# Kernel optimization log

Hardware: AMD Instinct MI355X
Metric: run time of the kernel (lower is better)

Reference implementation:

```python
import jax, jax.numpy as jnp
import numpy as np

D_K = 32  # hard-coded in original module


def setup_inputs() -> dict:
    key = jax.random.key(0)
    kq, kk, kv, km = jax.random.split(key, 4)
    B, H, S, D = 4, 12, 2048, D_K
    Q = jax.random.normal(kq, (B, H, S, D), dtype=jnp.float32)
    K = jax.random.normal(kk, (B, H, S, D), dtype=jnp.float32)
    V = jax.random.normal(kv, (B, H, S, D), dtype=jnp.float32)
    attn_mask = jax.random.bernoulli(km, 0.5, (B, H, S, S))
    return {"Q": Q, "K": K, "V": V, "attn_mask": attn_mask}


def tanh_max(a):
    # (exp(a) - exp(-a)) / sum_over_keys(exp(a) + exp(-a))
    ea = jnp.exp(a)
    ena = jnp.exp(-a)
    return (ea - ena) / (ea + ena).sum(axis=-1, keepdims=True)


def reference(Q, K, V, attn_mask):
    # scores: [B,H,S,S]
    scores = jnp.einsum("bhqd,bhkd->bhqk", Q, K) / np.sqrt(D_K).astype(np.float32)
    attn = tanh_max(scores)
    # NOTE: original calls attn.masked_fill(attn_mask, 0.0) WITHOUT assignment
    # (non-in-place), so the mask has no effect. Reproduced faithfully.
    context = jnp.einsum("bhqk,bhkd->bhqd", attn, V)
    return context
```

## Files before the change

### kernel.cpp

```cpp
#include <hip/hip_runtime.h>
#include <hip/hip_bf16.h>
#include <cstdint>
#include <cstddef>


#define SLEN 2048
#define DK   32
#define NBH  48
#define PROW 40

typedef __attribute__((ext_vector_type(8))) short bf16x8;
typedef __attribute__((ext_vector_type(4))) float f32x4;

__device__ __forceinline__ unsigned pk2(float a, float b) {
    __hip_bfloat162 h = __float22bfloat162_rn(make_float2(a, b));
    union { __hip_bfloat162 h2; unsigned u; } cv; cv.h2 = h; return cv.u;
}
__device__ __forceinline__ unsigned short f2b(float x) {
    __hip_bfloat16 h = __float2bfloat16(x);
    union { __hip_bfloat16 h; unsigned short u; } cv; cv.h = h; return cv.u;
}

__global__ __launch_bounds__(256)
void prep_vt(const float* __restrict__ V, unsigned short* __restrict__ VT) {
    __shared__ float tile[32][33];
    const int bh = blockIdx.x >> 6;
    const int kc = blockIdx.x & 63;
    const int t  = threadIdx.x;
    const int row = t >> 3, c4 = (t & 7) * 4;
    float4 v4 = *(const float4*)(V + ((size_t)bh * SLEN + kc * 32 + row) * DK + c4);
    tile[row][c4 + 0] = v4.x; tile[row][c4 + 1] = v4.y;
    tile[row][c4 + 2] = v4.z; tile[row][c4 + 3] = v4.w;
    __syncthreads();
    const int d = t >> 3, k4 = (t & 7) * 4;
    float a0 = tile[k4 + 0][d], a1 = tile[k4 + 1][d];
    float a2 = tile[k4 + 2][d], a3 = tile[k4 + 3][d];
    uint2 u; u.x = pk2(a0, a1); u.y = pk2(a2, a3);
    *(uint2*)(VT + ((size_t)bh * DK + d) * SLEN + kc * 32 + k4) = u;
}

__global__ __launch_bounds__(256, 4)
void attn_mfma(const float* __restrict__ Q, const float* __restrict__ K,
               const unsigned short* __restrict__ VT, float* __restrict__ Out) {
    __shared__ __align__(16) unsigned short Pbuf[4][16 * PROW];

    const int tid  = threadIdx.x;
    const int lane = tid & 63;
    const int wv   = tid >> 6;
    const int quad = lane >> 4;
    const int l16  = lane & 15;

    const int g     = blockIdx.x * 4 + wv;
    const int bh    = g >> 7;
    const int qbase = (g & 127) << 4;

    const float sc = 0.17677669529663687f * 1.4426950408889634f;
    const float* qp = Q + ((size_t)bh * SLEN + qbase + l16) * DK + quad * 8;
    float4 qa = *(const float4*)qp;
    float4 qb = *(const float4*)(qp + 4);
    union { bf16x8 v; unsigned u[4]; } aQ;
    aQ.u[0] = pk2(qa.x * sc, qa.y * sc); aQ.u[1] = pk2(qa.z * sc, qa.w * sc);
    aQ.u[2] = pk2(qb.x * sc, qb.y * sc); aQ.u[3] = pk2(qb.z * sc, qb.w * sc);

    f32x4 o0 = {0.f, 0.f, 0.f, 0.f};
    f32x4 o1 = {0.f, 0.f, 0.f, 0.f};
    const f32x4 zero = {0.f, 0.f, 0.f, 0.f};
    float den[4] = {0.f, 0.f, 0.f, 0.f};

    const float* kp = K + ((size_t)bh * SLEN + l16) * DK + quad * 8;
    const unsigned short* vp = VT + ((size_t)bh * DK + l16) * SLEN;
    unsigned short* pb = &Pbuf[wv][0];

    #pragma unroll 2
    for (int kb = 0; kb < SLEN; kb += 32) {
        const float* k0 = kp + (size_t)kb * DK;
        float4 ka = *(const float4*)k0,            kb4 = *(const float4*)(k0 + 4);
        float4 kc = *(const float4*)(k0 + 16*DK),  kd  = *(const float4*)(k0 + 16*DK + 4);
        union { bf16x8 v; unsigned u[4]; } bK0, bK1;
        bK0.u[0] = pk2(ka.x, ka.y);  bK0.u[1] = pk2(ka.z, ka.w);
        bK0.u[2] = pk2(kb4.x, kb4.y); bK0.u[3] = pk2(kb4.z, kb4.w);
        bK1.u[0] = pk2(kc.x, kc.y);  bK1.u[1] = pk2(kc.z, kc.w);
        bK1.u[2] = pk2(kd.x, kd.y);  bK1.u[3] = pk2(kd.z, kd.w);

        f32x4 s0 = __builtin_amdgcn_mfma_f32_16x16x32_bf16(aQ.v, bK0.v, zero, 0, 0, 0);
        f32x4 s1 = __builtin_amdgcn_mfma_f32_16x16x32_bf16(aQ.v, bK1.v, zero, 0, 0, 0);

        #pragma unroll
        for (int r = 0; r < 4; ++r) {
            float e0  = exp2f(s0[r]);
            float en0 = exp2f(-s0[r]);
            den[r] += e0 + en0;
            pb[(quad * 4 + r) * PROW + l16] = f2b(e0 - en0);
            float e1  = exp2f(s1[r]);
            float en1 = exp2f(-s1[r]);
            den[r] += e1 + en1;
            pb[(quad * 4 + r) * PROW + 16 + l16] = f2b(e1 - en1);
        }

        bf16x8 aP = *(const bf16x8*)(pb + l16 * PROW + quad * 8);

        bf16x8 bV0 = *(const bf16x8*)(vp + kb + quad * 8);
        bf16x8 bV1 = *(const bf16x8*)(vp + 16 * SLEN + kb + quad * 8);

        o0 = __builtin_amdgcn_mfma_f32_16x16x32_bf16(aP, bV0, o0, 0, 0, 0);
        o1 = __builtin_amdgcn_mfma_f32_16x16x32_bf16(aP, bV1, o1, 0, 0, 0);
    }

    #pragma unroll
    for (int r = 0; r < 4; ++r) {
        den[r] += __shfl_xor(den[r], 1, 16);
        den[r] += __shfl_xor(den[r], 2, 16);
        den[r] += __shfl_xor(den[r], 4, 16);
        den[r] += __shfl_xor(den[r], 8, 16);
    }

    float* outp = Out + ((size_t)bh * SLEN + qbase) * DK;
    #pragma unroll
    for (int r = 0; r < 4; ++r) {
        float inv = 1.0f / den[r];
        int q = quad * 4 + r;
        outp[(size_t)q * DK + l16]      = o0[r] * inv;
        outp[(size_t)q * DK + 16 + l16] = o1[r] * inv;
    }
}

extern "C" void kernel_launch(void* const* d_in, const int* in_sizes, int n_in,
                              void* d_out, int out_size, void* d_ws, size_t ws_size,
                              hipStream_t stream) {
    const float* Q = (const float*)d_in[0];
    const float* K = (const float*)d_in[1];
    const float* V = (const float*)d_in[2];
    float* Out = (float*)d_out;
    unsigned short* VT = (unsigned short*)d_ws;

    prep_vt<<<dim3(NBH * 64), dim3(256), 0, stream>>>(V, VT);
    attn_mfma<<<dim3(NBH * 32), dim3(256), 0, stream>>>(Q, K, VT, Out);
}
```

Measured before the change: 1.129 ms.

## Pre-pack K and V into MFMA fragment layout, prefetch and remap blocks per XCD

Adds a prep kernel that converts K to bf16 in a fragment-ordered layout and changes the V transpose to fragment order, so each lane in the attention loop reads one contiguous 16-byte vector per operand. The loop now software-prefetches the next chunk's K and V fragments, uses the raw exp2 builtin, and writes packed bf16 pairs to LDS. Blocks are remapped so that each XCD handles a contiguous set of heads, which should improve L2 reuse of K and V. The cost is an extra prep launch, more workspace, and more registers held for prefetched data.

Measured after the change: 934.3 us. 17.2% less time.

```diff
diff --git a/kernel.cpp b/kernel.cpp
--- a/kernel.cpp
+++ b/kernel.cpp
@@ -16,32 +16,49 @@
     __hip_bfloat162 h = __float22bfloat162_rn(make_float2(a, b));
     union { __hip_bfloat162 h2; unsigned u; } cv; cv.h2 = h; return cv.u;
 }
-__device__ __forceinline__ unsigned short f2b(float x) {
-    __hip_bfloat16 h = __float2bfloat16(x);
-    union { __hip_bfloat16 h; unsigned short u; } cv; cv.h = h; return cv.u;
+
+__global__ __launch_bounds__(256)
+void prep_k(const float* __restrict__ K, unsigned short* __restrict__ Kbf) {
+    const int b  = blockIdx.x;
+    const int bh = b >> 5, kg = b & 31;
+    const int tl = threadIdx.x >> 6, l = threadIdx.x & 63;
+    const int t  = kg * 4 + tl;
+    const int c  = t >> 1, tb = t & 1;
+    const int key = c * 32 + 2 * (l & 15) + tb;
+    const float* src = K + ((size_t)bh * SLEN + key) * DK + (l >> 4) * 8;
+    float4 a = *(const float4*)src;
+    float4 b4 = *(const float4*)(src + 4);
+    union { uint4 q; unsigned u[4]; } o;
+    o.u[0] = pk2(a.x, a.y);  o.u[1] = pk2(a.z, a.w);
+    o.u[2] = pk2(b4.x, b4.y); o.u[3] = pk2(b4.z, b4.w);
+    *(uint4*)(Kbf + (((size_t)bh * 128 + t) * 64 + l) * 8) = o.q;
 }
 
 __global__ __launch_bounds__(256)
-void prep_vt(const float* __restrict__ V, unsigned short* __restrict__ VT) {
+void prep_v(const float* __restrict__ V, unsigned short* __restrict__ VTf) {
     __shared__ float tile[32][33];
-    const int bh = blockIdx.x >> 6;
-    const int kc = blockIdx.x & 63;
+    const int b  = blockIdx.x;
+    const int bh = b >> 6, c = b & 63;
     const int t  = threadIdx.x;
-    const int row = t >> 3, c4 = (t & 7) * 4;
-    float4 v4 = *(const float4*)(V + ((size_t)bh * SLEN + kc * 32 + row) * DK + c4);
-    tile[row][c4 + 0] = v4.x; tile[row][c4 + 1] = v4.y;
-    tile[row][c4 + 2] = v4.z; tile[row][c4 + 3] = v4.w;
+    {
+        const int row = t >> 3, c4 = (t & 7) * 4;
+        float4 v4 = *(const float4*)(V + ((size_t)bh * SLEN + c * 32 + row) * DK + c4);
+        tile[row][c4 + 0] = v4.x; tile[row][c4 + 1] = v4.y;
+        tile[row][c4 + 2] = v4.z; tile[row][c4 + 3] = v4.w;
+    }
     __syncthreads();
-    const int d = t >> 3, k4 = (t & 7) * 4;
-    float a0 = tile[k4 + 0][d], a1 = tile[k4 + 1][d];
-    float a2 = tile[k4 + 2][d], a3 = tile[k4 + 3][d];
-    uint2 u; u.x = pk2(a0, a1); u.y = pk2(a2, a3);
-    *(uint2*)(VT + ((size_t)bh * DK + d) * SLEN + kc * 32 + k4) = u;
+    const int h = t >> 7, l = (t >> 1) & 63, jh = t & 1;
+    const int col = h * 16 + (l & 15);
+    const int r0  = (l >> 4) * 8 + jh * 4;
+    uint2 u;
+    u.x = pk2(tile[r0 + 0][col], tile[r0 + 1][col]);
+    u.y = pk2(tile[r0 + 2][col], tile[r0 + 3][col]);
+    *(uint2*)(VTf + ((((size_t)bh * 64 + c) * 2 + h) * 64 + l) * 8 + jh * 4) = u;
 }
 
 __global__ __launch_bounds__(256, 4)
-void attn_mfma(const float* __restrict__ Q, const float* __restrict__ K,
-               const unsigned short* __restrict__ VT, float* __restrict__ Out) {
+void attn_mfma(const float* __restrict__ Q, const unsigned short* __restrict__ Kbf,
+               const unsigned short* __restrict__ VTf, float* __restrict__ Out) {
     __shared__ __align__(16) unsigned short Pbuf[4][16 * PROW];
 
     const int tid  = threadIdx.x;
@@ -50,9 +67,12 @@
     const int quad = lane >> 4;
     const int l16  = lane & 15;
 
-    const int g     = blockIdx.x * 4 + wv;
-    const int bh    = g >> 7;
-    const int qbase = (g & 127) << 4;
+    const int b   = blockIdx.x;
+    const int xcd = b & 7;
+    const int i   = b >> 3;
+    const int bh  = xcd * 6 + (i % 6);
+    const int qt  = i / 6;
+    const int qbase = (qt * 4 + wv) * 16;
 
     const float sc = 0.17677669529663687f * 1.4426950408889634f;
     const float* qp = Q + ((size_t)bh * SLEN + qbase + l16) * DK + quad * 8;
@@ -62,48 +82,46 @@
     aQ.u[0] = pk2(qa.x * sc, qa.y * sc); aQ.u[1] = pk2(qa.z * sc, qa.w * sc);
     aQ.u[2] = pk2(qb.x * sc, qb.y * sc); aQ.u[3] = pk2(qb.z * sc, qb.w * sc);
 
+    const bf16x8* kf = (const bf16x8*)Kbf + (size_t)bh * 128 * 64 + lane;
+    const bf16x8* vf = (const bf16x8*)VTf + (size_t)bh * 128 * 64 + lane;
+
     f32x4 o0 = {0.f, 0.f, 0.f, 0.f};
     f32x4 o1 = {0.f, 0.f, 0.f, 0.f};
     const f32x4 zero = {0.f, 0.f, 0.f, 0.f};
     float den[4] = {0.f, 0.f, 0.f, 0.f};
 
-    const float* kp = K + ((size_t)bh * SLEN + l16) * DK + quad * 8;
-    const unsigned short* vp = VT + ((size_t)bh * DK + l16) * SLEN;
-    unsigned short* pb = &Pbuf[wv][0];
+    unsigned short* pb  = &Pbuf[wv][0];
+    unsigned*       pbw = (unsigned*)pb;
 
-    #pragma unroll 2
-    for (int kb = 0; kb < SLEN; kb += 32) {
-        const float* k0 = kp + (size_t)kb * DK;
-        float4 ka = *(const float4*)k0,            kb4 = *(const float4*)(k0 + 4);
-        float4 kc = *(const float4*)(k0 + 16*DK),  kd  = *(const float4*)(k0 + 16*DK + 4);
-        union { bf16x8 v; unsigned u[4]; } bK0, bK1;
-        bK0.u[0] = pk2(ka.x, ka.y);  bK0.u[1] = pk2(ka.z, ka.w);
-        bK0.u[2] = pk2(kb4.x, kb4.y); bK0.u[3] = pk2(kb4.z, kb4.w);
-        bK1.u[0] = pk2(kc.x, kc.y);  bK1.u[1] = pk2(kc.z, kc.w);
-        bK1.u[2] = pk2(kd.x, kd.y);  bK1.u[3] = pk2(kd.z, kd.w);
+    bf16x8 k0 = kf[0], k1 = kf[64];
+    bf16x8 v0 = vf[0], v1 = vf[64];
 
-        f32x4 s0 = __builtin_amdgcn_mfma_f32_16x16x32_bf16(aQ.v, bK0.v, zero, 0, 0, 0);
-        f32x4 s1 = __builtin_amdgcn_mfma_f32_16x16x32_bf16(aQ.v, bK1.v, zero, 0, 0, 0);
+    for (int c = 0; c < 64; ++c) {
+        const int cn = (c + 1) & 63;
+        bf16x8 nk0 = kf[(size_t)cn * 128];
+        bf16x8 nk1 = kf[(size_t)cn * 128 + 64];
+        bf16x8 nv0 = vf[(size_t)cn * 128];
+        bf16x8 nv1 = vf[(size_t)cn * 128 + 64];
+
+        f32x4 s0 = __builtin_amdgcn_mfma_f32_16x16x32_bf16(aQ.v, k0, zero, 0, 0, 0);
+        f32x4 s1 = __builtin_amdgcn_mfma_f32_16x16x32_bf16(aQ.v, k1, zero, 0, 0, 0);
 
         #pragma unroll
         for (int r = 0; r < 4; ++r) {
-            float e0  = exp2f(s0[r]);
-            float en0 = exp2f(-s0[r]);
-            den[r] += e0 + en0;
-            pb[(quad * 4 + r) * PROW + l16] = f2b(e0 - en0);
-            float e1  = exp2f(s1[r]);
-            float en1 = exp2f(-s1[r]);
-            den[r] += e1 + en1;
-            pb[(quad * 4 + r) * PROW + 16 + l16] = f2b(e1 - en1);
+            float e0  = __builtin_amdgcn_exp2f(s0[r]);
+            float en0 = __builtin_amdgcn_exp2f(-s0[r]);
+            float e1  = __builtin_amdgcn_exp2f(s1[r]);
+            float en1 = __builtin_amdgcn_exp2f(-s1[r]);
+            den[r] += (e0 + en0) + (e1 + en1);
+            pbw[(quad * 4 + r) * (PROW / 2) + l16] = pk2(e0 - en0, e1 - en1);
         }
 
         bf16x8 aP = *(const bf16x8*)(pb + l16 * PROW + quad * 8);
 
-        bf16x8 bV0 = *(const bf16x8*)(vp + kb + quad * 8);
-        bf16x8 bV1 = *(const bf16x8*)(vp + 16 * SLEN + kb + quad * 8);
+        o0 = __builtin_amdgcn_mfma_f32_16x16x32_bf16(aP, v0, o0, 0, 0, 0);
+        o1 = __builtin_amdgcn_mfma_f32_16x16x32_bf16(aP, v1, o1, 0, 0, 0);
 
-        o0 = __builtin_amdgcn_mfma_f32_16x16x32_bf16(aP, bV0, o0, 0, 0, 0);
-        o1 = __builtin_amdgcn_mfma_f32_16x16x32_bf16(aP, bV1, o1, 0, 0, 0);
+        k0 = nk0; k1 = nk1; v0 = nv0; v1 = nv1;
     }
 
     #pragma unroll
@@ -131,8 +149,10 @@
     const float* K = (const float*)d_in[1];
     const float* V = (const float*)d_in[2];
     float* Out = (float*)d_out;
-    unsigned short* VT = (unsigned short*)d_ws;
+    unsigned short* Kbf = (unsigned short*)d_ws;
+    unsigned short* VTf = Kbf + (size_t)NBH * SLEN * DK;
 
-    prep_vt<<<dim3(NBH * 64), dim3(256), 0, stream>>>(V, VT);
-    attn_mfma<<<dim3(NBH * 32), dim3(256), 0, stream>>>(Q, K, VT, Out);
+    prep_k<<<dim3(NBH * 32), dim3(256), 0, stream>>>(K, Kbf);
+    prep_v<<<dim3(NBH * 64), dim3(256), 0, stream>>>(V, VTf);
+    attn_mfma<<<dim3(NBH * 32), dim3(256), 0, stream>>>(Q, Kbf, VTf, Out);
 }
```
